# Kernel optimization log

Hardware: AMD Instinct MI355X
Metric: run time of the kernel (lower is better)

The kernel has to match this reference:

```python
import jax, jax.numpy as jnp
import numpy as np

B, F, V = 64, 256, 128   # groups, frames/group, vecs/group (uniform ragged groups)
CF = 512                 # cross_feature


def setup_inputs() -> dict:
    key = jax.random.key(0)
    ks = jax.random.split(key, 18)
    p = lambda k, s: jax.random.normal(k, s, jnp.float32) * 0.02
    return {
        "metas": jax.random.uniform(ks[0], (B, 5), jnp.float32),
        "meta_indexs": jnp.arange(B),
        "frames": jax.random.normal(ks[1], (B * F, 600), jnp.float32),
        "frame_indexs": jnp.repeat(jnp.arange(B), F),
        "vecs": jax.random.normal(ks[2], (B * V, 768), jnp.float32),
        "vec_indexs": jnp.repeat(jnp.arange(B), V),
        "audios": jax.random.normal(ks[3], (B, 128), jnp.float32),
        "audio_indexs": jnp.arange(B),
        "Wfk": p(ks[4], (CF, 600)), "Wfv": p(ks[5], (CF, 600)),
        "Wvk": p(ks[6], (CF, 768)), "Wvv": p(ks[7], (CF, 768)),
        "Wav": p(ks[8], (CF, 128)),
        "Wff_f": p(ks[9], (2, CF, CF)),
        "Wff_v": p(ks[10], (2, CF, CF)),
        "Wff_a": p(ks[11], (2, CF, CF)),
        "Wout1": p(ks[12], (768, 3 * CF + 3)),
        "Wout2": p(ks[13], (512, 768)),
        "Wout3": p(ks[14], (64, 512)),
        "Wout4": p(ks[15], (1, 64)),
    }


def reference(metas, meta_indexs, frames, frame_indexs, vecs, vec_indexs,
              audios, audio_indexs, Wfk, Wfv, Wvk, Wvv, Wav,
              Wff_f, Wff_v, Wff_a, Wout1, Wout2, Wout3, Wout4):
    # groups are uniform: reshape ragged rows into [B, n, d] (indexes are
    # contiguous repeats per setup_inputs, so the mask-gathers become reshapes)
    b = audios.shape[0]
    fb = frames.reshape(b, -1, frames.shape[-1])   # [B,F,600]
    vb = vecs.reshape(b, -1, vecs.shape[-1])       # [B,V,768]
    relu = jax.nn.relu

    f_k = relu(jnp.einsum('bfd,cd->bfc', fb, Wfk))     # [B,F,CF]
    f_v = relu(jnp.einsum('bfd,cd->bfc', fb, Wfv))
    v_k = relu(jnp.einsum('bvd,cd->bvc', vb, Wvk))     # [B,V,CF]
    v_v = relu(jnp.einsum('bvd,cd->bvc', vb, Wvv))
    a_v = relu(audios @ Wav.T)                         # [B,CF]

    # torch: softmax(mm(k, q)) with no dim on an (N,1) tensor -> dim=1 -> ones,
    # so the initial "attended" queries are plain sums of the value projections.
    f_q_p = f_v.sum(axis=1)                            # [B,CF]
    v_q_p = v_v.sum(axis=1)
    a_q_p = a_v                                        # single audio row

    for i in range(2):
        attn_f = jax.nn.softmax(jnp.einsum('bfc,bc->bf', f_k, v_q_p) / CF, axis=1)
        f_c = jnp.einsum('bf,bfc->bc', attn_f, f_v)
        f_q_n = f_c @ Wff_f[i].T + f_q_p
        attn_v = jax.nn.softmax(jnp.einsum('bvc,bc->bv', v_k, v_q_p) / CF, axis=1)
        v_c = jnp.einsum('bv,bvc->bc', attn_v, v_v)
        v_q_n = v_c @ Wff_v[i].T + v_q_p
        # audio attention is softmax over a single element -> weight 1
        a_q_n = a_v @ Wff_a[i].T + a_q_p
        f_q_p, v_q_p, a_q_p = f_q_n, v_q_n, a_q_n      # dropout is dead code

    mean = a_q_p.mean(axis=1, keepdims=True)
    std = a_q_p.std(axis=1, keepdims=True, ddof=1)     # torch.std is unbiased
    na = (a_q_p - mean) / std

    goal = metas[:, 1:2] / 1500.0
    dura = metas[:, 3:4] - metas[:, 2:3]
    dura = jnp.where(dura > 8000.0, 100.0, dura) / 100.0
    create = metas[:, 4:5] / 5.0

    feats = jnp.concatenate([f_q_p, v_q_p, na, goal, create, dura], axis=1)  # [B,1539]
    h = relu(feats @ Wout1.T)
    h = relu(h @ Wout2.T)
    h = relu(h @ Wout3.T)
    out = jax.nn.sigmoid(h @ Wout4.T)                  # [B,1]
    return out[:, 0]
```

## Files before the change

kernel.cpp:

```cpp
#include <hip/hip_runtime.h>
#include <hip/hip_bf16.h>

typedef __attribute__((ext_vector_type(4))) float f32x4;
typedef __attribute__((ext_vector_type(8))) __bf16 bf16x8;
typedef __attribute__((ext_vector_type(8))) unsigned short us8;
typedef __attribute__((ext_vector_type(4))) unsigned int u32x4;

#define LDS_AS __attribute__((address_space(3)))
#define GLB_AS __attribute__((address_space(1)))

__device__ __forceinline__ float bf2f(unsigned short h) {
    return __builtin_bit_cast(float, (unsigned)h << 16);
}
__device__ __forceinline__ unsigned short f2bf(float f) {
    return __builtin_bit_cast(unsigned short, (__bf16)f);
}
__device__ __forceinline__ us8 cvt8(f32x4 a, f32x4 b) {
    bf16x8 r;
    r[0] = (__bf16)a[0]; r[1] = (__bf16)a[1]; r[2] = (__bf16)a[2]; r[3] = (__bf16)a[3];
    r[4] = (__bf16)b[0]; r[5] = (__bf16)b[1]; r[6] = (__bf16)b[2]; r[7] = (__bf16)b[3];
    return __builtin_bit_cast(us8, r);
}
__device__ __forceinline__ void cp16(const void* g, void* l) {
    __builtin_amdgcn_global_load_lds((const GLB_AS unsigned int*)g,
                                     (LDS_AS unsigned int*)l, 16, 0, 0);
}

__global__ __launch_bounds__(256) void prep_kernel(
    const float* __restrict__ frames, const float* __restrict__ Wfk, const float* __restrict__ Wfv,
    const float* __restrict__ vecs, const float* __restrict__ Wvk, const float* __restrict__ Wvv,
    const float* __restrict__ Wout1, const float* __restrict__ audios, const float* __restrict__ Wav,
    unsigned short* __restrict__ fbf, unsigned short* __restrict__ wf,
    unsigned short* __restrict__ vbf, unsigned short* __restrict__ wv,
    float* __restrict__ W1p, float* __restrict__ zbase,
    float* __restrict__ a_v, float* __restrict__ a_q_p)
{
    const int t = threadIdx.x;
    int bid = blockIdx.x;
    if (bid < 1216) {
        #pragma unroll
        for (int j = 0; j < 4; ++j) {
            int i = bid * 256 + t + j * (1216 * 256);
            int row = i / 76, k = (i - row * 76) * 8;
            us8 o = {0, 0, 0, 0, 0, 0, 0, 0};
            if (k < 600) {
                const float* s = frames + (size_t)row * 600 + k;
                o = cvt8(*(const f32x4*)s, *(const f32x4*)(s + 4));
            }
            *(us8*)(fbf + (size_t)row * 608 + k) = o;
        }
        return;
    }
    bid -= 1216;
    if (bid < 76) {
        #pragma unroll
        for (int j = 0; j < 4; ++j) {
            int i = bid * 256 + t + j * (76 * 256);
            int row = i / 76, k = (i - row * 76) * 8;
            const float* src = row < 512 ? Wfk + (size_t)row * 600 : Wfv + (size_t)(row - 512) * 600;
            us8 o = {0, 0, 0, 0, 0, 0, 0, 0};
            if (k < 600) o = cvt8(*(const f32x4*)(src + k), *(const f32x4*)(src + k + 4));
            *(us8*)(wf + (size_t)row * 608 + k) = o;
        }
        return;
    }
    bid -= 76;
    if (bid < 768) {
        #pragma unroll
        for (int j = 0; j < 4; ++j) {
            int i = bid * 256 + t + j * (768 * 256);
            int row = i / 96, k = (i - row * 96) * 8;
            const float* s = vecs + (size_t)row * 768 + k;
            *(us8*)(vbf + (size_t)row * 768 + k) = cvt8(*(const f32x4*)s, *(const f32x4*)(s + 4));
        }
        return;
    }
    bid -= 768;
    if (bid < 96) {
        #pragma unroll
        for (int j = 0; j < 4; ++j) {
            int i = bid * 256 + t + j * (96 * 256);
            int row = i / 96, k = (i - row * 96) * 8;
            const float* src = (row < 512 ? Wvk + (size_t)row * 768
                                          : Wvv + (size_t)(row - 512) * 768) + k;
            *(us8*)(wv + (size_t)row * 768 + k) = cvt8(*(const f32x4*)src, *(const f32x4*)(src + 4));
        }
        return;
    }
    bid -= 96;
    if (bid < 336) {
        #pragma unroll
        for (int j = 0; j < 4; ++j) {
            int i = bid * 256 + t + j * (336 * 256);
            int r = i / 448, k = (i - r * 448) * 4;
            f32x4 o;
            #pragma unroll
            for (int q = 0; q < 4; ++q) {
                int kk = k + q;
                o[q] = kk < 1539 ? Wout1[(size_t)r * 1539 + kk] : 0.f;
            }
            *(f32x4*)(W1p + (size_t)r * 1792 + k) = o;
        }
        return;
    }
    bid -= 336;
    if (bid < 36) {
        f32x4 z = {0, 0, 0, 0};
        #pragma unroll
        for (int j = 0; j < 4; ++j) {
            int i = bid * 256 + t + j * (36 * 256);
            *(f32x4*)(zbase + (size_t)i * 4) = z;
        }
        return;
    }
    bid -= 36;
    {
        __shared__ float aud[128];
        const int b = bid;
        if (t < 128) aud[t] = audios[b * 128 + t];
        __syncthreads();
        #pragma unroll
        for (int cc = 0; cc < 2; ++cc) {
            int c = 2 * t + cc;
            const float* wr = Wav + (size_t)c * 128;
            float s = 0.f;
            #pragma unroll
            for (int k4 = 0; k4 < 32; ++k4) {
                f32x4 wvv = *(const f32x4*)(wr + k4 * 4);
                s += wvv[0] * aud[k4 * 4] + wvv[1] * aud[k4 * 4 + 1]
                   + wvv[2] * aud[k4 * 4 + 2] + wvv[3] * aud[k4 * 4 + 3];
            }
            s = s > 0.f ? s : 0.f;
            a_v[b * 512 + c] = s;
            a_q_p[b * 512 + c] = s;
        }
    }
}

__global__ __launch_bounds__(256) void gemm_bt_relu(
    const unsigned short* __restrict__ Af, const unsigned short* __restrict__ Bf,
    unsigned short* __restrict__ Cfo, float* __restrict__ qf,
    const unsigned short* __restrict__ Av, const unsigned short* __restrict__ Bv,
    unsigned short* __restrict__ Cvo, float* __restrict__ qv)
{
    __shared__ alignas(16) unsigned short sA[3][4096];
    __shared__ alignas(16) unsigned short sB[3][4096];
    const int t = threadIdx.x;
    const int w = t >> 6, l = t & 63;
    const unsigned short *A, *B;
    unsigned short* C;
    float* qout;
    int Kp, ktiles, gshift, nwg, pb;
    if (blockIdx.x < 1024) { A = Af; B = Bf; C = Cfo; qout = qf; Kp = 608; ktiles = 19; gshift = 8; nwg = 1024; pb = blockIdx.x; }
    else                   { A = Av; B = Bv; C = Cvo; qout = qv; Kp = 768; ktiles = 24; gshift = 7; nwg = 512;  pb = blockIdx.x - 1024; }
    const int swz = (pb & 7) * (nwg >> 3) + (pb >> 3);
    const int bm = swz >> 3, bn = swz & 7;
    const int m0 = bm << 7, n0 = bn << 7;

    const int srow = t >> 2;
    const int schunk = (t & 3) ^ ((t >> 2) & 3);
    const unsigned short* gA = A + (size_t)(m0 + srow) * Kp + (schunk << 3);
    const unsigned short* gB = B + (size_t)(n0 + srow) * Kp + (schunk << 3);

    const int wr = w >> 1, wc = w & 1;
    const int rsw = (((l >> 4) ^ (l & 3)) << 3);
    const int fAoff = (wr * 64 + (l & 15)) * 32 + rsw;
    const int fBoff = (wc * 64 + (l & 15)) * 32 + rsw;

    auto stage = [&](int buf, int kt) {
        char* lA = (char*)(&sA[buf][0]) + w * 1024;
        char* lB = (char*)(&sB[buf][0]) + w * 1024;
        const unsigned short* ga = gA + kt * 32;
        const unsigned short* gb = gB + kt * 32;
        cp16(ga, lA);
        cp16(ga + (size_t)64 * Kp, lA + 4096);
        cp16(gb, lB);
        cp16(gb + (size_t)64 * Kp, lB + 4096);
    };

    stage(0, 0);
    stage(1, 1);
    f32x4 acc[4][4] = {};
    int cur = 0;
    for (int kt = 0; kt < ktiles; ++kt) {
        if (kt + 1 < ktiles) {
            asm volatile("s_waitcnt vmcnt(4)" ::: "memory");
        } else {
            asm volatile("s_waitcnt vmcnt(0)" ::: "memory");
        }
        __builtin_amdgcn_sched_barrier(0);
        __builtin_amdgcn_s_barrier();
        __builtin_amdgcn_sched_barrier(0);

        bf16x8 af[4], bfr[4];
        #pragma unroll
        for (int i = 0; i < 4; ++i) {
            af[i]  = *(const bf16x8*)(&sA[cur][0] + fAoff + i * 512);
            bfr[i] = *(const bf16x8*)(&sB[cur][0] + fBoff + i * 512);
        }
        #pragma unroll
        for (int mi = 0; mi < 4; ++mi)
            #pragma unroll
            for (int ni = 0; ni < 4; ++ni)
                acc[mi][ni] = __builtin_amdgcn_mfma_f32_16x16x32_bf16(af[mi], bfr[ni], acc[mi][ni], 0, 0, 0);

        if (kt + 2 < ktiles) {
            int b2 = cur + 2; if (b2 >= 3) b2 -= 3;
            stage(b2, kt + 2);
        }
        cur = (cur + 1 == 3) ? 0 : cur + 1;
    }

    const int crow0 = m0 + wr * 64 + ((l >> 4) << 2);
    const int ccol0 = n0 + wc * 64 + (l & 15);
    #pragma unroll
    for (int mi = 0; mi < 4; ++mi)
        #pragma unroll
        for (int ni = 0; ni < 4; ++ni)
            #pragma unroll
            for (int j = 0; j < 4; ++j) {
                float v = acc[mi][ni][j];
                v = v > 0.f ? v : 0.f;
                C[(size_t)(crow0 + mi * 16 + j) * 1024 + (ccol0 + ni * 16)] = f2bf(v);
            }
    if (n0 >= 512) {
        const int g = m0 >> gshift;
        float csum[4];
        #pragma unroll
        for (int ni = 0; ni < 4; ++ni) {
            float s = 0.f;
            #pragma unroll
            for (int mi = 0; mi < 4; ++mi)
                #pragma unroll
                for (int j = 0; j < 4; ++j)
                    s += fmaxf(acc[mi][ni][j], 0.f);
            s += __shfl_xor(s, 16, 64);
            s += __shfl_xor(s, 32, 64);
            csum[ni] = s;
        }
        if (l < 16) {
            #pragma unroll
            for (int ni = 0; ni < 4; ++ni)
                atomicAdd(&qout[g * 512 + (ccol0 - 512) + ni * 16], csum[ni]);
        }
    }
}

__global__ __launch_bounds__(256) void scores_kernel(
    const unsigned short* __restrict__ Cf, const unsigned short* __restrict__ Cv,
    const float* __restrict__ v_q_p, float* __restrict__ sbuf, float* __restrict__ fvz)
{
    const int t = threadIdx.x, bid = blockIdx.x;
    if (bid < 64) {
        f32x4 z = {0, 0, 0, 0};
        ((f32x4*)fvz)[bid * 256 + t] = z;
    }
    const int w = t >> 6, l = t & 63;
    int fbase, g, soff;
    const unsigned short* X;
    if (bid < 1024) { fbase = bid * 16 + w * 4; g = fbase >> 8; X = Cf; soff = 0; }
    else            { fbase = (bid - 1024) * 16 + w * 4; g = fbase >> 7; X = Cv; soff = 16384; }
    const float* vq = v_q_p + g * 512 + l * 8;
    f32x4 q0 = *(const f32x4*)vq;
    f32x4 q1 = *(const f32x4*)(vq + 4);
    #pragma unroll
    for (int i = 0; i < 4; ++i) {
        const int frame = fbase + i;
        u32x4 u = *(const u32x4*)(X + (size_t)frame * 1024 + l * 8);
        float acc = q0[0] * bf2f((unsigned short)(u[0] & 0xffff)) + q0[1] * bf2f((unsigned short)(u[0] >> 16))
                  + q0[2] * bf2f((unsigned short)(u[1] & 0xffff)) + q0[3] * bf2f((unsigned short)(u[1] >> 16))
                  + q1[0] * bf2f((unsigned short)(u[2] & 0xffff)) + q1[1] * bf2f((unsigned short)(u[2] >> 16))
                  + q1[2] * bf2f((unsigned short)(u[3] & 0xffff)) + q1[3] * bf2f((unsigned short)(u[3] >> 16));
        #pragma unroll
        for (int m = 1; m < 64; m <<= 1) acc += __shfl_xor(acc, m, 64);
        if (l == 0) sbuf[soff + frame] = acc * (1.f / 512.f);
    }
}

__global__ __launch_bounds__(256) void pv_kernel(
    const unsigned short* __restrict__ Cf, const unsigned short* __restrict__ Cv,
    const float* __restrict__ sbuf, float* __restrict__ fc, float* __restrict__ vc)
{
    __shared__ float ws[256];
    __shared__ float red[256];
    const int t = threadIdx.x, bid = blockIdx.x;
    int g, chunk, NF, soff;
    const unsigned short* X;
    float* outp;
    if (bid < 1024) { g = bid >> 4; chunk = bid & 15; NF = 256; X = Cf; soff = g * 256; outp = fc; }
    else { int b2 = bid - 1024; g = b2 >> 3; chunk = b2 & 7; NF = 128; X = Cv; soff = 16384 + g * 128; outp = vc; }
    float s = (t < NF) ? sbuf[soff + t] : -1e30f;
    red[t] = s;
    __syncthreads();
    for (int st = 128; st > 0; st >>= 1) { if (t < st) red[t] = fmaxf(red[t], red[t + st]); __syncthreads(); }
    float m = red[0];
    __syncthreads();
    float e = (t < NF) ? __expf(s - m) : 0.f;
    ws[t] = e;
    red[t] = e;
    __syncthreads();
    for (int st = 128; st > 0; st >>= 1) { if (t < st) red[t] += red[t + st]; __syncthreads(); }
    float inv = 1.f / red[0];
    const int f0 = g * NF + chunk * 16;
    const unsigned int* q = (const unsigned int*)X + (size_t)f0 * 512 + 256 + t;
    float s0 = 0.f, s1 = 0.f;
    #pragma unroll 4
    for (int f = 0; f < 16; ++f) {
        float a = ws[chunk * 16 + f];
        unsigned u = q[(size_t)f * 512];
        s0 += a * bf2f((unsigned short)(u & 0xffff));
        s1 += a * bf2f((unsigned short)(u >> 16));
    }
    atomicAdd(&outp[g * 512 + 2 * t],     s0 * inv);
    atomicAdd(&outp[g * 512 + 2 * t + 1], s1 * inv);
}

__device__ __forceinline__ void gemv_body(
    const float* __restrict__ X, int ldx, int dorelu,
    const float* __restrict__ W, int ldw, float* __restrict__ Y, int ldy,
    int nc, int kc, int bc)
{
    __shared__ float xs[4096];
    const int t = threadIdx.x;
    #pragma unroll
    for (int j = 0; j < 16; ++j) {
        int idx = t + j * 256;
        float v = X[(size_t)(bc * 32 + (idx >> 7)) * ldx + kc * 128 + (idx & 127)];
        xs[idx] = dorelu ? (v > 0.f ? v : 0.f) : v;
    }
    __syncthreads();
    const int r = t & 63, bg = t >> 6;
    const int row = nc * 64 + r;
    const float* wrow = W + (size_t)row * ldw + kc * 128;
    float acc[8] = {};
    #pragma unroll 8
    for (int k4 = 0; k4 < 32; ++k4) {
        f32x4 wvv = *(const f32x4*)(wrow + k4 * 4);
        #pragma unroll
        for (int bb = 0; bb < 8; ++bb) {
            f32x4 xv = *(const f32x4*)(xs + (bg * 8 + bb) * 128 + k4 * 4);
            acc[bb] += wvv[0] * xv[0] + wvv[1] * xv[1] + wvv[2] * xv[2] + wvv[3] * xv[3];
        }
    }
    #pragma unroll
    for (int bb = 0; bb < 8; ++bb)
        atomicAdd(&Y[(size_t)(bc * 32 + bg * 8 + bb) * ldy + row], acc[bb]);
}

__global__ __launch_bounds__(256) void update_kernel(
    const float* __restrict__ Wff_f, const float* __restrict__ Wff_v, const float* __restrict__ Wff_a,
    int iter, const float* __restrict__ fc, const float* __restrict__ vc, const float* __restrict__ a_v,
    float* __restrict__ f_q_p, float* __restrict__ v_q_p, float* __restrict__ a_q_p)
{
    int id = blockIdx.x;
    const int op = id >> 6; id &= 63;
    const int nc = id & 7, kc = (id >> 3) & 3, bc = id >> 5;
    const float* W = (op == 0 ? Wff_f : op == 1 ? Wff_v : Wff_a) + (size_t)iter * 262144;
    const float* X = op == 0 ? fc : op == 1 ? vc : a_v;
    float* Y = op == 0 ? f_q_p : op == 1 ? v_q_p : a_q_p;
    gemv_body(X, 512, 0, W, 512, Y, 512, nc, kc, bc);
}

__global__ __launch_bounds__(256) void gemvb_kernel(
    const float* __restrict__ X, int ldx, int dorelu,
    const float* __restrict__ W, int ldw, float* __restrict__ Y, int ldy,
    int NC, int KC)
{
    int bid = blockIdx.x;
    const int nc = bid % NC; bid /= NC;
    const int kc = bid % KC;
    const int bc = bid / KC;
    gemv_body(X, ldx, dorelu, W, ldw, Y, ldy, nc, kc, bc);
}

__global__ __launch_bounds__(512) void normfeats_kernel(
    const float* __restrict__ a_q_p, const float* __restrict__ f_q_p, const float* __restrict__ v_q_p,
    const float* __restrict__ metas, float* __restrict__ feats)
{
    __shared__ float red[512];
    const int t = threadIdx.x, b = blockIdx.x;
    float a = a_q_p[b * 512 + t];
    red[t] = a;
    __syncthreads();
    for (int s = 256; s > 0; s >>= 1) { if (t < s) red[t] += red[t + s]; __syncthreads(); }
    float mean = red[0] * (1.f / 512.f);
    __syncthreads();
    float d = a - mean;
    red[t] = d * d;
    __syncthreads();
    for (int s = 256; s > 0; s >>= 1) { if (t < s) red[t] += red[t + s]; __syncthreads(); }
    float sd = sqrtf(red[0] * (1.f / 511.f));
    float* fr = feats + (size_t)b * 1792;
    fr[t]        = f_q_p[b * 512 + t];
    fr[512 + t]  = v_q_p[b * 512 + t];
    fr[1024 + t] = d / sd;
    if (t < 256) {
        float v = 0.f;
        if (t == 0) v = metas[b * 5 + 1] * (1.f / 1500.f);
        else if (t == 1) v = metas[b * 5 + 4] * 0.2f;
        else if (t == 2) {
            float du = metas[b * 5 + 3] - metas[b * 5 + 2];
            v = (du > 8000.f ? 100.f : du) * 0.01f;
        }
        fr[1536 + t] = v;
    }
}

__global__ __launch_bounds__(256) void mlp34_kernel(
    const float* __restrict__ h2acc, const float* __restrict__ W3, const float* __restrict__ W4,
    float* __restrict__ out)
{
    __shared__ float xs[512];
    __shared__ float part[256];
    __shared__ float h3[64];
    const int t = threadIdx.x, b = blockIdx.x;
    {
        float v0 = h2acc[(size_t)b * 512 + t];
        float v1 = h2acc[(size_t)b * 512 + 256 + t];
        xs[t] = v0 > 0.f ? v0 : 0.f;
        xs[256 + t] = v1 > 0.f ? v1 : 0.f;
    }
    __syncthreads();
    const int r = t & 63, q = t >> 6;
    const float* wrow = W3 + (size_t)r * 512 + q * 128;
    float acc = 0.f;
    #pragma unroll 8
    for (int k4 = 0; k4 < 32; ++k4) {
        f32x4 wvv = *(const f32x4*)(wrow + k4 * 4);
        f32x4 xv  = *(const f32x4*)(xs + q * 128 + k4 * 4);
        acc += wvv[0] * xv[0] + wvv[1] * xv[1] + wvv[2] * xv[2] + wvv[3] * xv[3];
    }
    part[t] = acc;
    __syncthreads();
    if (t < 64) {
        float h = part[t] + part[t + 64] + part[t + 128] + part[t + 192];
        h3[t] = h > 0.f ? h : 0.f;
    }
    __syncthreads();
    if (t < 64) {
        float v = h3[t] * W4[t];
        #pragma unroll
        for (int m = 1; m < 64; m <<= 1) v += __shfl_xor(v, m, 64);
        if (t == 0) out[b] = 1.f / (1.f + __expf(-v));
    }
}

extern "C" void kernel_launch(void* const* d_in, const int* in_sizes, int n_in,
                              void* d_out, int out_size, void* d_ws, size_t ws_size,
                              hipStream_t stream)
{
    const float* metas  = (const float*)d_in[0];
    const float* frames = (const float*)d_in[2];
    const float* vecs   = (const float*)d_in[4];
    const float* audios = (const float*)d_in[6];
    const float* Wfk   = (const float*)d_in[8];
    const float* Wfv   = (const float*)d_in[9];
    const float* Wvk   = (const float*)d_in[10];
    const float* Wvv   = (const float*)d_in[11];
    const float* Wav   = (const float*)d_in[12];
    const float* Wff_f = (const float*)d_in[13];
    const float* Wff_v = (const float*)d_in[14];
    const float* Wff_a = (const float*)d_in[15];
    const float* Wout1 = (const float*)d_in[16];
    const float* Wout2 = (const float*)d_in[17];
    const float* Wout3 = (const float*)d_in[18];
    const float* Wout4 = (const float*)d_in[19];
    float* out = (float*)d_out;

    char* p = (char*)d_ws;
    auto alloc = [&](size_t n) { char* r = p; p += (n + 255) & ~(size_t)255; return r; };
    unsigned short* fbf = (unsigned short*)alloc(16384ull * 608 * 2);
    unsigned short* wf  = (unsigned short*)alloc(1024ull * 608 * 2);
    unsigned short* vbf = (unsigned short*)alloc(8192ull * 768 * 2);
    unsigned short* wv  = (unsigned short*)alloc(1024ull * 768 * 2);
    unsigned short* Cf  = (unsigned short*)alloc(16384ull * 1024 * 2);
    unsigned short* Cv  = (unsigned short*)alloc(8192ull * 1024 * 2);
    float* W1p   = (float*)alloc(768ull * 1792 * 4);
    float* feats = (float*)alloc(64ull * 1792 * 4);
    float* hacc  = (float*)alloc(81920ull * 4);
    float* qbuf  = (float*)alloc(2ull * 64 * 512 * 4);
    float* h1acc = hacc;
    float* h2acc = hacc + 64 * 768;
    float* f_q_p = qbuf;
    float* v_q_p = qbuf + 64 * 512;
    float* a_q_p = (float*)alloc(64ull * 512 * 4);
    float* a_v   = (float*)alloc(64ull * 512 * 4);
    float* fvc   = (float*)alloc(2ull * 64 * 512 * 4);
    float* fcb   = fvc;
    float* vcb   = fvc + 64 * 512;
    float* sbuf  = (float*)alloc(24576ull * 4);

    prep_kernel<<<2592, 256, 0, stream>>>(frames, Wfk, Wfv, vecs, Wvk, Wvv, Wout1,
                                          audios, Wav, fbf, wf, vbf, wv, W1p, hacc,
                                          a_v, a_q_p);
    gemm_bt_relu<<<1536, 256, 0, stream>>>(fbf, wf, Cf, f_q_p, vbf, wv, Cv, v_q_p);
    for (int i = 0; i < 2; ++i) {
        scores_kernel<<<1536, 256, 0, stream>>>(Cf, Cv, v_q_p, sbuf, fvc);
        pv_kernel<<<1536, 256, 0, stream>>>(Cf, Cv, sbuf, fcb, vcb);
        update_kernel<<<192, 256, 0, stream>>>(Wff_f, Wff_v, Wff_a, i, fcb, vcb, a_v,
                                               f_q_p, v_q_p, a_q_p);
    }
    normfeats_kernel<<<64, 512, 0, stream>>>(a_q_p, f_q_p, v_q_p, metas, feats);
    gemvb_kernel<<<336, 256, 0, stream>>>(feats, 1792, 0, W1p, 1792, h1acc, 768, 12, 14);
    gemvb_kernel<<<96, 256, 0, stream>>>(h1acc, 768, 1, Wout2, 768, h2acc, 512, 8, 6);
    mlp34_kernel<<<64, 256, 0, stream>>>(h2acc, Wout3, Wout4, out);
}
```

Measured before the change: 175.2 us.

## Restructure GEMM pipeline into paired k-tile rounds with double-buffered pairs, drop LDS swizzle

Replaces the 3-stage per-k-tile pipeline with rounds of two k-tiles, double-buffered across 4 LDS slots. Each round waits on all outstanding loads, then issues the next pair's prefetch before computing. This halves the number of barriers and waitcnts per k-loop. It also removes the XOR swizzle on the global-to-LDS chunk placement and fragment reads, which risks LDS bank conflicts. The larger LDS footprint (64KB per block) may reduce occupancy.

```diff
diff --git a/kernel.cpp b/kernel.cpp
--- a/kernel.cpp
+++ b/kernel.cpp
@@ -143,8 +143,8 @@
     const unsigned short* __restrict__ Av, const unsigned short* __restrict__ Bv,
     unsigned short* __restrict__ Cvo, float* __restrict__ qv)
 {
-    __shared__ alignas(16) unsigned short sA[3][4096];
-    __shared__ alignas(16) unsigned short sB[3][4096];
+    __shared__ alignas(16) unsigned short sA[4][4096];
+    __shared__ alignas(16) unsigned short sB[4][4096];
     const int t = threadIdx.x;
     const int w = t >> 6, l = t & 63;
     const unsigned short *A, *B;
@@ -157,17 +157,15 @@
     const int bm = swz >> 3, bn = swz & 7;
     const int m0 = bm << 7, n0 = bn << 7;
 
-    const int srow = t >> 2;
-    const int schunk = (t & 3) ^ ((t >> 2) & 3);
-    const unsigned short* gA = A + (size_t)(m0 + srow) * Kp + (schunk << 3);
-    const unsigned short* gB = B + (size_t)(n0 + srow) * Kp + (schunk << 3);
+    const int srow = t >> 2, sk0 = (t & 3) << 3;
+    const unsigned short* gA = A + (size_t)(m0 + srow) * Kp + sk0;
+    const unsigned short* gB = B + (size_t)(n0 + srow) * Kp + sk0;
 
     const int wr = w >> 1, wc = w & 1;
-    const int rsw = (((l >> 4) ^ (l & 3)) << 3);
-    const int fAoff = (wr * 64 + (l & 15)) * 32 + rsw;
-    const int fBoff = (wc * 64 + (l & 15)) * 32 + rsw;
-
-    auto stage = [&](int buf, int kt) {
+    const int fAoff = (wr * 64 + (l & 15)) * 32 + ((l >> 4) << 3);
+    const int fBoff = (wc * 64 + (l & 15)) * 32 + ((l >> 4) << 3);
+
+    auto stage1 = [&](int buf, int kt) {
         char* lA = (char*)(&sA[buf][0]) + w * 1024;
         char* lB = (char*)(&sB[buf][0]) + w * 1024;
         const unsigned short* ga = gA + kt * 32;
@@ -177,38 +175,38 @@
         cp16(gb, lB);
         cp16(gb + (size_t)64 * Kp, lB + 4096);
     };
-
-    stage(0, 0);
-    stage(1, 1);
+    auto stage2 = [&](int pair, int t0) {
+        stage1(pair * 2, t0);
+        if (t0 + 1 < ktiles) stage1(pair * 2 + 1, t0 + 1);
+    };
+
+    const int R = (ktiles + 1) >> 1;
+    stage2(0, 0);
     f32x4 acc[4][4] = {};
-    int cur = 0;
-    for (int kt = 0; kt < ktiles; ++kt) {
-        if (kt + 1 < ktiles) {
-            asm volatile("s_waitcnt vmcnt(4)" ::: "memory");
-        } else {
-            asm volatile("s_waitcnt vmcnt(0)" ::: "memory");
-        }
+    for (int r = 0; r < R; ++r) {
+        asm volatile("s_waitcnt vmcnt(0)" ::: "memory");
         __builtin_amdgcn_sched_barrier(0);
         __builtin_amdgcn_s_barrier();
         __builtin_amdgcn_sched_barrier(0);
-
-        bf16x8 af[4], bfr[4];
-        #pragma unroll
-        for (int i = 0; i < 4; ++i) {
-            af[i]  = *(const bf16x8*)(&sA[cur][0] + fAoff + i * 512);
-            bfr[i] = *(const bf16x8*)(&sB[cur][0] + fBoff + i * 512);
-        }
-        #pragma unroll
-        for (int mi = 0; mi < 4; ++mi)
-            #pragma unroll
-            for (int ni = 0; ni < 4; ++ni)
-                acc[mi][ni] = __builtin_amdgcn_mfma_f32_16x16x32_bf16(af[mi], bfr[ni], acc[mi][ni], 0, 0, 0);
-
-        if (kt + 2 < ktiles) {
-            int b2 = cur + 2; if (b2 >= 3) b2 -= 3;
-            stage(b2, kt + 2);
-        }
-        cur = (cur + 1 == 3) ? 0 : cur + 1;
+        if (r + 1 < R) stage2((r + 1) & 1, 2 * (r + 1));
+
+        const int pb2 = (r & 1) * 2;
+        #pragma unroll
+        for (int s = 0; s < 2; ++s) {
+            if (2 * r + s < ktiles) {
+                bf16x8 af[4], bfr[4];
+                #pragma unroll
+                for (int i = 0; i < 4; ++i) {
+                    af[i]  = *(const bf16x8*)(&sA[pb2 + s][0] + fAoff + i * 512);
+                    bfr[i] = *(const bf16x8*)(&sB[pb2 + s][0] + fBoff + i * 512);
+                }
+                #pragma unroll
+                for (int mi = 0; mi < 4; ++mi)
+                    #pragma unroll
+                    for (int ni = 0; ni < 4; ++ni)
+                        acc[mi][ni] = __builtin_amdgcn_mfma_f32_16x16x32_bf16(af[mi], bfr[ni], acc[mi][ni], 0, 0, 0);
+            }
+        }
     }
 
     const int crow0 = m0 + wr * 64 + ((l >> 4) << 2);
```

After: 179.5 us. +2.5%, slower.

## Fuse attention iterations and MLP tail into one cooperative persistent kernel

Applied to the files above, without the earlier changes.

Replaces the ten small launches (scores, pv, update twice, then normfeats, two gemvs, mlp34) with one cooperative kernel of 512 blocks that loops over work units and separates phases with grid-wide syncs. The aim is to remove per-launch overhead and tail gaps between many short kernels. The normfeats stage is reworked to use 256 threads instead of 512. The GEMM's LDS XOR swizzle is also removed, which may bring back LDS bank conflicts. Grid syncs add their own cost, and the cooperative launch requires all 512 blocks to be co-resident.

```diff
diff --git a/kernel.cpp b/kernel.cpp
--- a/kernel.cpp
+++ b/kernel.cpp
@@ -1,5 +1,8 @@
 #include <hip/hip_runtime.h>
 #include <hip/hip_bf16.h>
+#include <hip/hip_cooperative_groups.h>
+
+namespace cg = cooperative_groups;
 
 typedef __attribute__((ext_vector_type(4))) float f32x4;
 typedef __attribute__((ext_vector_type(8))) __bf16 bf16x8;
@@ -157,15 +160,13 @@
     const int bm = swz >> 3, bn = swz & 7;
     const int m0 = bm << 7, n0 = bn << 7;
 
-    const int srow = t >> 2;
-    const int schunk = (t & 3) ^ ((t >> 2) & 3);
-    const unsigned short* gA = A + (size_t)(m0 + srow) * Kp + (schunk << 3);
-    const unsigned short* gB = B + (size_t)(n0 + srow) * Kp + (schunk << 3);
+    const int srow = t >> 2, sk0 = (t & 3) << 3;
+    const unsigned short* gA = A + (size_t)(m0 + srow) * Kp + sk0;
+    const unsigned short* gB = B + (size_t)(n0 + srow) * Kp + sk0;
 
     const int wr = w >> 1, wc = w & 1;
-    const int rsw = (((l >> 4) ^ (l & 3)) << 3);
-    const int fAoff = (wr * 64 + (l & 15)) * 32 + rsw;
-    const int fBoff = (wc * 64 + (l & 15)) * 32 + rsw;
+    const int fAoff = (wr * 64 + (l & 15)) * 32 + ((l >> 4) << 3);
+    const int fBoff = (wc * 64 + (l & 15)) * 32 + ((l >> 4) << 3);
 
     auto stage = [&](int buf, int kt) {
         char* lA = (char*)(&sA[buf][0]) + w * 1024;
@@ -246,49 +247,49 @@
     }
 }
 
-__global__ __launch_bounds__(256) void scores_kernel(
-    const unsigned short* __restrict__ Cf, const unsigned short* __restrict__ Cv,
-    const float* __restrict__ v_q_p, float* __restrict__ sbuf, float* __restrict__ fvz)
-{
-    const int t = threadIdx.x, bid = blockIdx.x;
-    if (bid < 64) {
+__device__ __forceinline__ void scores_body(
+    int u, const unsigned short* Cf, const unsigned short* Cv,
+    const float* v_q_p, float* sbuf, float* fvz)
+{
+    const int t = threadIdx.x;
+    if (u < 64) {
         f32x4 z = {0, 0, 0, 0};
-        ((f32x4*)fvz)[bid * 256 + t] = z;
+        ((f32x4*)fvz)[u * 256 + t] = z;
     }
     const int w = t >> 6, l = t & 63;
     int fbase, g, soff;
     const unsigned short* X;
-    if (bid < 1024) { fbase = bid * 16 + w * 4; g = fbase >> 8; X = Cf; soff = 0; }
-    else            { fbase = (bid - 1024) * 16 + w * 4; g = fbase >> 7; X = Cv; soff = 16384; }
+    if (u < 1024) { fbase = u * 16 + w * 4; g = fbase >> 8; X = Cf; soff = 0; }
+    else          { fbase = (u - 1024) * 16 + w * 4; g = fbase >> 7; X = Cv; soff = 16384; }
     const float* vq = v_q_p + g * 512 + l * 8;
     f32x4 q0 = *(const f32x4*)vq;
     f32x4 q1 = *(const f32x4*)(vq + 4);
     #pragma unroll
     for (int i = 0; i < 4; ++i) {
         const int frame = fbase + i;
-        u32x4 u = *(const u32x4*)(X + (size_t)frame * 1024 + l * 8);
-        float acc = q0[0] * bf2f((unsigned short)(u[0] & 0xffff)) + q0[1] * bf2f((unsigned short)(u[0] >> 16))
-                  + q0[2] * bf2f((unsigned short)(u[1] & 0xffff)) + q0[3] * bf2f((unsigned short)(u[1] >> 16))
-                  + q1[0] * bf2f((unsigned short)(u[2] & 0xffff)) + q1[1] * bf2f((unsigned short)(u[2] >> 16))
-                  + q1[2] * bf2f((unsigned short)(u[3] & 0xffff)) + q1[3] * bf2f((unsigned short)(u[3] >> 16));
+        u32x4 uu = *(const u32x4*)(X + (size_t)frame * 1024 + l * 8);
+        float acc = q0[0] * bf2f((unsigned short)(uu[0] & 0xffff)) + q0[1] * bf2f((unsigned short)(uu[0] >> 16))
+                  + q0[2] * bf2f((unsigned short)(uu[1] & 0xffff)) + q0[3] * bf2f((unsigned short)(uu[1] >> 16))
+                  + q1[0] * bf2f((unsigned short)(uu[2] & 0xffff)) + q1[1] * bf2f((unsigned short)(uu[2] >> 16))
+                  + q1[2] * bf2f((unsigned short)(uu[3] & 0xffff)) + q1[3] * bf2f((unsigned short)(uu[3] >> 16));
         #pragma unroll
         for (int m = 1; m < 64; m <<= 1) acc += __shfl_xor(acc, m, 64);
         if (l == 0) sbuf[soff + frame] = acc * (1.f / 512.f);
     }
 }
 
-__global__ __launch_bounds__(256) void pv_kernel(
-    const unsigned short* __restrict__ Cf, const unsigned short* __restrict__ Cv,
-    const float* __restrict__ sbuf, float* __restrict__ fc, float* __restrict__ vc)
-{
-    __shared__ float ws[256];
-    __shared__ float red[256];
-    const int t = threadIdx.x, bid = blockIdx.x;
+__device__ __forceinline__ void pv_body(
+    int u, const unsigned short* Cf, const unsigned short* Cv,
+    const float* sbuf, float* fc, float* vc, float* smem)
+{
+    float* ws  = smem;
+    float* red = smem + 256;
+    const int t = threadIdx.x;
     int g, chunk, NF, soff;
     const unsigned short* X;
     float* outp;
-    if (bid < 1024) { g = bid >> 4; chunk = bid & 15; NF = 256; X = Cf; soff = g * 256; outp = fc; }
-    else { int b2 = bid - 1024; g = b2 >> 3; chunk = b2 & 7; NF = 128; X = Cv; soff = 16384 + g * 128; outp = vc; }
+    if (u < 1024) { g = u >> 4; chunk = u & 15; NF = 256; X = Cf; soff = g * 256; outp = fc; }
+    else { int b2 = u - 1024; g = b2 >> 3; chunk = b2 & 7; NF = 128; X = Cv; soff = 16384 + g * 128; outp = vc; }
     float s = (t < NF) ? sbuf[soff + t] : -1e30f;
     red[t] = s;
     __syncthreads();
@@ -307,20 +308,20 @@
     #pragma unroll 4
     for (int f = 0; f < 16; ++f) {
         float a = ws[chunk * 16 + f];
-        unsigned u = q[(size_t)f * 512];
-        s0 += a * bf2f((unsigned short)(u & 0xffff));
-        s1 += a * bf2f((unsigned short)(u >> 16));
+        unsigned uu = q[(size_t)f * 512];
+        s0 += a * bf2f((unsigned short)(uu & 0xffff));
+        s1 += a * bf2f((unsigned short)(uu >> 16));
     }
     atomicAdd(&outp[g * 512 + 2 * t],     s0 * inv);
     atomicAdd(&outp[g * 512 + 2 * t + 1], s1 * inv);
+    __syncthreads();
 }
 
 __device__ __forceinline__ void gemv_body(
     const float* __restrict__ X, int ldx, int dorelu,
     const float* __restrict__ W, int ldw, float* __restrict__ Y, int ldy,
-    int nc, int kc, int bc)
-{
-    __shared__ float xs[4096];
+    int nc, int kc, int bc, float* xs)
+{
     const int t = threadIdx.x;
     #pragma unroll
     for (int j = 0; j < 16; ++j) {
@@ -345,75 +346,51 @@
     #pragma unroll
     for (int bb = 0; bb < 8; ++bb)
         atomicAdd(&Y[(size_t)(bc * 32 + bg * 8 + bb) * ldy + row], acc[bb]);
-}
-
-__global__ __launch_bounds__(256) void update_kernel(
-    const float* __restrict__ Wff_f, const float* __restrict__ Wff_v, const float* __restrict__ Wff_a,
-    int iter, const float* __restrict__ fc, const float* __restrict__ vc, const float* __restrict__ a_v,
-    float* __restrict__ f_q_p, float* __restrict__ v_q_p, float* __restrict__ a_q_p)
-{
-    int id = blockIdx.x;
-    const int op = id >> 6; id &= 63;
-    const int nc = id & 7, kc = (id >> 3) & 3, bc = id >> 5;
-    const float* W = (op == 0 ? Wff_f : op == 1 ? Wff_v : Wff_a) + (size_t)iter * 262144;
-    const float* X = op == 0 ? fc : op == 1 ? vc : a_v;
-    float* Y = op == 0 ? f_q_p : op == 1 ? v_q_p : a_q_p;
-    gemv_body(X, 512, 0, W, 512, Y, 512, nc, kc, bc);
-}
-
-__global__ __launch_bounds__(256) void gemvb_kernel(
-    const float* __restrict__ X, int ldx, int dorelu,
-    const float* __restrict__ W, int ldw, float* __restrict__ Y, int ldy,
-    int NC, int KC)
-{
-    int bid = blockIdx.x;
-    const int nc = bid % NC; bid /= NC;
-    const int kc = bid % KC;
-    const int bc = bid / KC;
-    gemv_body(X, ldx, dorelu, W, ldw, Y, ldy, nc, kc, bc);
-}
-
-__global__ __launch_bounds__(512) void normfeats_kernel(
-    const float* __restrict__ a_q_p, const float* __restrict__ f_q_p, const float* __restrict__ v_q_p,
-    const float* __restrict__ metas, float* __restrict__ feats)
-{
-    __shared__ float red[512];
-    const int t = threadIdx.x, b = blockIdx.x;
-    float a = a_q_p[b * 512 + t];
-    red[t] = a;
-    __syncthreads();
-    for (int s = 256; s > 0; s >>= 1) { if (t < s) red[t] += red[t + s]; __syncthreads(); }
+    __syncthreads();
+}
+
+__device__ __forceinline__ void normfeats_body(
+    int b, const float* a_q_p, const float* f_q_p, const float* v_q_p,
+    const float* metas, float* feats, float* red)
+{
+    const int t = threadIdx.x;
+    float a0 = a_q_p[b * 512 + t];
+    float a1 = a_q_p[b * 512 + 256 + t];
+    red[t] = a0 + a1;
+    __syncthreads();
+    for (int s = 128; s > 0; s >>= 1) { if (t < s) red[t] += red[t + s]; __syncthreads(); }
     float mean = red[0] * (1.f / 512.f);
     __syncthreads();
-    float d = a - mean;
-    red[t] = d * d;
-    __syncthreads();
-    for (int s = 256; s > 0; s >>= 1) { if (t < s) red[t] += red[t + s]; __syncthreads(); }
+    float d0 = a0 - mean, d1 = a1 - mean;
+    red[t] = d0 * d0 + d1 * d1;
+    __syncthreads();
+    for (int s = 128; s > 0; s >>= 1) { if (t < s) red[t] += red[t + s]; __syncthreads(); }
     float sd = sqrtf(red[0] * (1.f / 511.f));
+    __syncthreads();
     float* fr = feats + (size_t)b * 1792;
-    fr[t]        = f_q_p[b * 512 + t];
-    fr[512 + t]  = v_q_p[b * 512 + t];
-    fr[1024 + t] = d / sd;
-    if (t < 256) {
-        float v = 0.f;
-        if (t == 0) v = metas[b * 5 + 1] * (1.f / 1500.f);
-        else if (t == 1) v = metas[b * 5 + 4] * 0.2f;
-        else if (t == 2) {
-            float du = metas[b * 5 + 3] - metas[b * 5 + 2];
-            v = (du > 8000.f ? 100.f : du) * 0.01f;
-        }
-        fr[1536 + t] = v;
-    }
-}
-
-__global__ __launch_bounds__(256) void mlp34_kernel(
-    const float* __restrict__ h2acc, const float* __restrict__ W3, const float* __restrict__ W4,
-    float* __restrict__ out)
-{
-    __shared__ float xs[512];
-    __shared__ float part[256];
-    __shared__ float h3[64];
-    const int t = threadIdx.x, b = blockIdx.x;
+    fr[t]         = f_q_p[b * 512 + t];
+    fr[256 + t]   = f_q_p[b * 512 + 256 + t];
+    fr[512 + t]   = v_q_p[b * 512 + t];
+    fr[768 + t]   = v_q_p[b * 512 + 256 + t];
+    fr[1024 + t]  = d0 / sd;
+    fr[1280 + t]  = d1 / sd;
+    float v = 0.f;
+    if (t == 0) v = metas[b * 5 + 1] * (1.f / 1500.f);
+    else if (t == 1) v = metas[b * 5 + 4] * 0.2f;
+    else if (t == 2) {
+        float du = metas[b * 5 + 3] - metas[b * 5 + 2];
+        v = (du > 8000.f ? 100.f : du) * 0.01f;
+    }
+    fr[1536 + t] = v;
+}
+
+__device__ __forceinline__ void mlp34_body(
+    int b, const float* h2acc, const float* W3, const float* W4, float* out, float* smem)
+{
+    float* xs   = smem;
+    float* part = smem + 512;
+    float* h3   = smem + 768;
+    const int t = threadIdx.x;
     {
         float v0 = h2acc[(size_t)b * 512 + t];
         float v1 = h2acc[(size_t)b * 512 + 256 + t];
@@ -443,6 +420,61 @@
         for (int m = 1; m < 64; m <<= 1) v += __shfl_xor(v, m, 64);
         if (t == 0) out[b] = 1.f / (1.f + __expf(-v));
     }
+    __syncthreads();
+}
+
+struct MidArgs {
+    const unsigned short* Cf;
+    const unsigned short* Cv;
+    const float* Wff_f; const float* Wff_v; const float* Wff_a;
+    const float* metas; const float* Wout2; const float* Wout3; const float* Wout4;
+    const float* a_v;
+    float* f_q_p; float* v_q_p; float* a_q_p;
+    float* sbuf; float* fvc; float* feats;
+    const float* W1p; float* h1acc; float* h2acc; float* out;
+};
+
+__global__ __launch_bounds__(256, 2) void mid_kernel(MidArgs A)
+{
+    __shared__ float smem[4096];
+    cg::grid_group grid = cg::this_grid();
+    const int nb = gridDim.x;
+    float* fcb = A.fvc;
+    float* vcb = A.fvc + 64 * 512;
+
+    for (int it = 0; it < 2; ++it) {
+        for (int u = blockIdx.x; u < 1536; u += nb)
+            scores_body(u, A.Cf, A.Cv, A.v_q_p, A.sbuf, A.fvc);
+        grid.sync();
+        for (int u = blockIdx.x; u < 1536; u += nb)
+            pv_body(u, A.Cf, A.Cv, A.sbuf, fcb, vcb, smem);
+        grid.sync();
+        for (int u = blockIdx.x; u < 192; u += nb) {
+            int id = u;
+            const int op = id >> 6; id &= 63;
+            const int nc = id & 7, kc = (id >> 3) & 3, bc = id >> 5;
+            const float* W = (op == 0 ? A.Wff_f : op == 1 ? A.Wff_v : A.Wff_a) + (size_t)it * 262144;
+            const float* X = op == 0 ? fcb : op == 1 ? vcb : A.a_v;
+            float* Y = op == 0 ? A.f_q_p : op == 1 ? A.v_q_p : A.a_q_p;
+            gemv_body(X, 512, 0, W, 512, Y, 512, nc, kc, bc, smem);
+        }
+        grid.sync();
+    }
+    for (int u = blockIdx.x; u < 64; u += nb)
+        normfeats_body(u, A.a_q_p, A.f_q_p, A.v_q_p, A.metas, A.feats, smem);
+    grid.sync();
+    for (int u = blockIdx.x; u < 336; u += nb) {
+        int nc = u % 12, kc = (u / 12) % 14, bc = u / 168;
+        gemv_body(A.feats, 1792, 0, A.W1p, 1792, A.h1acc, 768, nc, kc, bc, smem);
+    }
+    grid.sync();
+    for (int u = blockIdx.x; u < 96; u += nb) {
+        int nc = u % 8, kc = (u / 8) % 6, bc = u / 48;
+        gemv_body(A.h1acc, 768, 1, A.Wout2, 768, A.h2acc, 512, nc, kc, bc, smem);
+    }
+    grid.sync();
+    for (int u = blockIdx.x; u < 64; u += nb)
+        mlp34_body(u, A.h2acc, A.Wout3, A.Wout4, A.out, smem);
 }
 
 extern "C" void kernel_launch(void* const* d_in, const int* in_sizes, int n_in,
@@ -486,22 +518,22 @@
     float* a_q_p = (float*)alloc(64ull * 512 * 4);
     float* a_v   = (float*)alloc(64ull * 512 * 4);
     float* fvc   = (float*)alloc(2ull * 64 * 512 * 4);
-    float* fcb   = fvc;
-    float* vcb   = fvc + 64 * 512;
     float* sbuf  = (float*)alloc(24576ull * 4);
 
     prep_kernel<<<2592, 256, 0, stream>>>(frames, Wfk, Wfv, vecs, Wvk, Wvv, Wout1,
                                           audios, Wav, fbf, wf, vbf, wv, W1p, hacc,
                                           a_v, a_q_p);
     gemm_bt_relu<<<1536, 256, 0, stream>>>(fbf, wf, Cf, f_q_p, vbf, wv, Cv, v_q_p);
-    for (int i = 0; i < 2; ++i) {
-        scores_kernel<<<1536, 256, 0, stream>>>(Cf, Cv, v_q_p, sbuf, fvc);
-        pv_kernel<<<1536, 256, 0, stream>>>(Cf, Cv, sbuf, fcb, vcb);
-        update_kernel<<<192, 256, 0, stream>>>(Wff_f, Wff_v, Wff_a, i, fcb, vcb, a_v,
-                                               f_q_p, v_q_p, a_q_p);
-    }
-    normfeats_kernel<<<64, 512, 0, stream>>>(a_q_p, f_q_p, v_q_p, metas, feats);
-    gemvb_kernel<<<336, 256, 0, stream>>>(feats, 1792, 0, W1p, 1792, h1acc, 768, 12, 14);
-    gemvb_kernel<<<96, 256, 0, stream>>>(h1acc, 768, 1, Wout2, 768, h2acc, 512, 8, 6);
-    mlp34_kernel<<<64, 256, 0, stream>>>(h2acc, Wout3, Wout4, out);
-}
+
+    MidArgs margs;
+    margs.Cf = Cf; margs.Cv = Cv;
+    margs.Wff_f = Wff_f; margs.Wff_v = Wff_v; margs.Wff_a = Wff_a;
+    margs.metas = metas; margs.Wout2 = Wout2; margs.Wout3 = Wout3; margs.Wout4 = Wout4;
+    margs.a_v = a_v;
+    margs.f_q_p = f_q_p; margs.v_q_p = v_q_p; margs.a_q_p = a_q_p;
+    margs.sbuf = sbuf; margs.fvc = fvc; margs.feats = feats;
+    margs.W1p = W1p; margs.h1acc = h1acc; margs.h2acc = h2acc; margs.out = out;
+    void* kargs[] = { &margs };
+    hipLaunchCooperativeKernel(reinterpret_cast<void*>(mid_kernel),
+                               dim3(512), dim3(256), kargs, 0, stream);
+}
```

New measurement: 673.5 us. 284% more time.
